# Kernel tuning notes

Hardware: AMD Instinct MI355X
Metric: run time of the kernel (lower is better)

The kernel has to match this reference:

```python
import jax, jax.numpy as jnp
import numpy as np

D_MODEL = 1024
N_HEADS = 16
D_K = D_MODEL // N_HEADS
B, T = 2, 2048


def setup_inputs() -> dict:
    key = jax.random.key(0)
    ks = jax.random.split(key, 9)
    s = 1.0 / np.sqrt(D_MODEL)
    def lin(kw, kb):
        W = jax.random.uniform(kw, (D_MODEL, D_MODEL), jnp.float32, -s, s)
        b = jax.random.uniform(kb, (D_MODEL,), jnp.float32, -s, s)
        return W, b
    Wq, bq = lin(ks[0], ks[1])
    Wk, bk = lin(ks[2], ks[3])
    Wv, bv = lin(ks[4], ks[5])
    Wo, bo = lin(ks[6], ks[7])
    x = jax.random.normal(ks[8], (B, T, D_MODEL), jnp.float32)
    return {"x": x, "Wq": Wq, "bq": bq, "Wk": Wk, "bk": bk,
            "Wv": Wv, "bv": bv, "Wo": Wo, "bo": bo}


def reference(x, Wq, bq, Wk, bk, Wv, bv, Wo, bo):
    Bn, Tn, _ = x.shape
    # torch Linear: x @ W.T + b
    def proj(W, b):
        y = x @ W.T + b  # [B, T, D]
        return y.reshape(Bn, Tn, N_HEADS, D_K).transpose(0, 2, 1, 3)  # [B, H, T, d_k]
    q = proj(Wq, bq)
    k = proj(Wk, bk)
    v = proj(Wv, bv)
    scores = jnp.einsum('bhqd,bhkd->bhqk', q, k) / jnp.sqrt(jnp.float32(D_K))
    causal = jnp.tril(jnp.ones((Tn, Tn), dtype=bool))  # True = keep
    scores = jnp.where(causal[None, None], scores, -jnp.inf)
    attn = jax.nn.softmax(scores, axis=-1)
    # dropout is identity in eval mode
    ctx = jnp.einsum('bhqk,bhkd->bhqd', attn, v)
    ctx = ctx.transpose(0, 2, 1, 3).reshape(Bn, Tn, D_MODEL)
    return ctx @ Wo.T + bo
```

## Files before the change

### kernel.cpp

```cpp
#include <hip/hip_runtime.h>
#include <hip/hip_bf16.h>
#include <stdint.h>

#define D_MODEL 1024
#define NH 16
#define DK 64
#define BB 2
#define TT 2048
#define NROWS (BB*TT)

typedef short bf16x8 __attribute__((ext_vector_type(8)));
typedef short bf16x4 __attribute__((ext_vector_type(4)));
typedef float f32x4  __attribute__((ext_vector_type(4)));

#if __has_builtin(__builtin_amdgcn_mfma_f32_16x16x16_bf16)
  #define MFMA16(a,b,c) __builtin_amdgcn_mfma_f32_16x16x16_bf16(a,b,c,0,0,0)
  #define HAVE_M16 1
#elif __has_builtin(__builtin_amdgcn_mfma_f32_16x16x16bf16_1k)
  #define MFMA16(a,b,c) __builtin_amdgcn_mfma_f32_16x16x16bf16_1k(a,b,c,0,0,0)
  #define HAVE_M16 1
#else
  #define HAVE_M16 0
#endif

#if __has_builtin(__builtin_amdgcn_global_load_lds)
  #define HAVE_GLDS 1
__device__ __forceinline__ void gload16(const unsigned short* g, unsigned short* lds){
    __builtin_amdgcn_global_load_lds(
        (const __attribute__((address_space(1))) unsigned int*)g,
        (__attribute__((address_space(3))) unsigned int*)lds, 16, 0, 0);
}
#else
  #define HAVE_GLDS 0
#endif

__device__ __forceinline__ unsigned pkbf(float a, float b){
    float2 t; t.x = a; t.y = b;
    __hip_bfloat162 h = __float22bfloat162_rn(t);
    return *reinterpret_cast<unsigned*>(&h);
}
__device__ __forceinline__ unsigned short bfbits(float a){
    __hip_bfloat16 h = __float2bfloat16(a);
    return *reinterpret_cast<unsigned short*>(&h);
}

__global__ __launch_bounds__(256) void conv_all(
    const float* __restrict__ x,
    const float* __restrict__ Wq, const float* __restrict__ Wk,
    const float* __restrict__ Wv, const float* __restrict__ Wo,
    unsigned short* __restrict__ xb, unsigned short* __restrict__ wb)
{
    const int blk = blockIdx.x;
    const float* src; unsigned short* dst; size_t i;
    if (blk < 2048) {
        src = x; dst = xb;
        i = ((size_t)blk * 256 + threadIdx.x) * 8;
    } else {
        const int t = (blk - 2048) >> 9;
        src = (t == 0) ? Wq : (t == 1) ? Wk : (t == 2) ? Wv : Wo;
        dst = wb + (size_t)t * D_MODEL * D_MODEL;
        i = ((size_t)((blk - 2048) & 511) * 256 + threadIdx.x) * 8;
    }
    float4 a = *(const float4*)(src + i);
    float4 b = *(const float4*)(src + i + 4);
    uint4 w;
    w.x = pkbf(a.x, a.y); w.y = pkbf(a.z, a.w);
    w.z = pkbf(b.x, b.y); w.w = pkbf(b.z, b.w);
    *(uint4*)(dst + i) = w;
}

__global__ __launch_bounds__(256) void conv_bf16(
    const float* __restrict__ x, unsigned short* __restrict__ y)
{
    size_t i = ((size_t)blockIdx.x * 256 + threadIdx.x) * 8;
    float4 a = *(const float4*)(x + i);
    float4 b = *(const float4*)(x + i + 4);
    uint4 w;
    w.x = pkbf(a.x, a.y); w.y = pkbf(a.z, a.w);
    w.z = pkbf(b.x, b.y); w.w = pkbf(b.z, b.w);
    *(uint4*)(y + i) = w;
}

#if HAVE_GLDS
template<int MI, int NB, bool CF32>
__device__ __forceinline__ void gemm_async(
    const unsigned short* __restrict__ Ap, const unsigned short* __restrict__ Bp,
    const float* __restrict__ bias, void* __restrict__ Cp,
    bool vt, float scale, unsigned short* As, unsigned short* Bs)
{
    constexpr int BMt = MI * 32, BNt = NB * 32;
    const int K = D_MODEL, N = D_MODEL;
    const int tid  = threadIdx.x;
    const int m0   = blockIdx.y * BMt;
    const int n0   = blockIdx.x * BNt;
    const int lane = tid & 63;
    const int w    = tid >> 6;
    const int wm   = (w >> 1) * (MI * 16);
    const int wn   = (w &  1) * (BNt / 2);
    const int l16  = lane & 15;
    const int quad = lane >> 4;
    const int crow = lane >> 2;
    const int ccol = (lane & 3) * 8;

    constexpr int CA = MI / 2;
    constexpr int CB = NB / 2;

    auto issue = [&](int buf, int k0){
        #pragma unroll
        for (int c = 0; c < CA; ++c) {
            const int chunk = w * CA + c;
            gload16(Ap + (size_t)(m0 + chunk*16 + crow) * K + k0 + ccol,
                    As + buf * BMt * 32 + chunk * 512);
        }
        #pragma unroll
        for (int c = 0; c < CB; ++c) {
            const int chunk = w * CB + c;
            gload16(Bp + (size_t)(n0 + chunk*16 + crow) * K + k0 + ccol,
                    Bs + buf * BNt * 32 + chunk * 512);
        }
    };

    f32x4 acc[MI][NB] = {};
    issue(0, 0);

    constexpr int ITER = D_MODEL / 32;
    for (int it = 0; it < ITER; ++it) {
        __syncthreads();
        if (it + 1 < ITER) issue((it + 1) & 1, (it + 1) * 32);
        const unsigned short* A = As + (it & 1) * BMt * 32;
        const unsigned short* B = Bs + (it & 1) * BNt * 32;
        bf16x8 af[MI], bg[NB];
        #pragma unroll
        for (int i = 0; i < MI; ++i)
            af[i] = *(const bf16x8*)&A[(wm + 16*i + l16) * 32 + quad * 8];
        #pragma unroll
        for (int j = 0; j < NB; ++j)
            bg[j] = *(const bf16x8*)&B[(wn + 16*j + l16) * 32 + quad * 8];
        #pragma unroll
        for (int i = 0; i < MI; ++i)
            #pragma unroll
            for (int j = 0; j < NB; ++j)
                acc[i][j] = __builtin_amdgcn_mfma_f32_16x16x32_bf16(af[i], bg[j], acc[i][j], 0, 0, 0);
    }

    #pragma unroll
    for (int j = 0; j < NB; ++j) {
        const int n = n0 + wn + 16*j + l16;
        const float bj = bias[n];
        #pragma unroll
        for (int i = 0; i < MI; ++i) {
            const int m = m0 + wm + 16*i + quad*4;
            if (vt) {
                const int b = m >> 11, t = m & 2047;
                ushort4 wv;
                wv.x = bfbits(acc[i][j][0] + bj);
                wv.y = bfbits(acc[i][j][1] + bj);
                wv.z = bfbits(acc[i][j][2] + bj);
                wv.w = bfbits(acc[i][j][3] + bj);
                *(ushort4*)((unsigned short*)Cp + (size_t)b * D_MODEL * TT
                            + (size_t)n * TT + t) = wv;
            } else {
                #pragma unroll
                for (int r = 0; r < 4; ++r) {
                    float v = (acc[i][j][r] + bj) * scale;
                    if (CF32) ((float*)Cp)[(size_t)(m + r) * N + n] = v;
                    else      ((__hip_bfloat16*)Cp)[(size_t)(m + r) * N + n] = __float2bfloat16(v);
                }
            }
        }
    }
}
#endif

#define ASTR 40

template<int MI, int NB, bool AF32, bool BF32, bool CF32>
__device__ __forceinline__ void gemm_body(
    const void* __restrict__ Ap, const void* __restrict__ Bp,
    const float* __restrict__ bias, void* __restrict__ Cp,
    bool vt, float scale, unsigned short* As, unsigned short* Bs)
{
    constexpr int BMt = MI * 32, BNt = NB * 32;
    const int K = D_MODEL, N = D_MODEL;
    const int tid  = threadIdx.x;
    const int m0   = blockIdx.y * BMt;
    const int n0   = blockIdx.x * BNt;
    const int lane = tid & 63;
    const int wave = tid >> 6;
    const int wm   = (wave >> 1) * (MI * 16);
    const int wn   = (wave &  1) * (BNt / 2);
    const int l16  = lane & 15;
    const int quad = lane >> 4;
    const int ar = (MI == 4) ? (tid >> 1) : (tid >> 2);
    const int ac = (MI == 4) ? ((tid & 1) * 16) : ((tid & 3) * 8);
    const int br = (NB == 4) ? (tid >> 1) : (tid >> 2);
    const int bc = (NB == 4) ? ((tid & 1) * 16) : ((tid & 3) * 8);

    uint4 pa[4], pb[4];

    auto loadA = [&](int k0){
        if (AF32) {
            const float* p = (const float*)Ap + (size_t)(m0 + ar) * K + k0 + ac;
            pa[0] = *(const uint4*)(p);     pa[1] = *(const uint4*)(p + 4);
            if (MI == 4) { pa[2] = *(const uint4*)(p + 8); pa[3] = *(const uint4*)(p + 12); }
        } else {
            const unsigned short* p = (const unsigned short*)Ap + (size_t)(m0 + ar) * K + k0 + ac;
            pa[0] = *(const uint4*)(p);
            if (MI == 4) pa[1] = *(const uint4*)(p + 8);
        }
    };
    auto loadB = [&](int k0){
        if (BF32) {
            const float* p = (const float*)Bp + (size_t)(n0 + br) * K + k0 + bc;
            pb[0] = *(const uint4*)(p); pb[1] = *(const uint4*)(p + 4);
            if (NB == 4) { pb[2] = *(const uint4*)(p + 8); pb[3] = *(const uint4*)(p + 12); }
        } else {
            const unsigned short* p = (const unsigned short*)Bp + (size_t)(n0 + br) * K + k0 + bc;
            pb[0] = *(const uint4*)(p);
            if (NB == 4) pb[1] = *(const uint4*)(p + 8);
        }
    };
    auto stage = [&](int buf){
        unsigned short* A = As + buf * BMt * ASTR;
        unsigned short* B = Bs + buf * BNt * ASTR;
        if (AF32) {
            const float* f = (const float*)pa;
            uint4 w0;
            w0.x = pkbf(f[0], f[1]); w0.y = pkbf(f[2], f[3]);
            w0.z = pkbf(f[4], f[5]); w0.w = pkbf(f[6], f[7]);
            *(uint4*)&A[ar*ASTR + ac] = w0;
            if (MI == 4) {
                uint4 w1;
                w1.x = pkbf(f[8], f[9]);   w1.y = pkbf(f[10], f[11]);
                w1.z = pkbf(f[12], f[13]); w1.w = pkbf(f[14], f[15]);
                *(uint4*)&A[ar*ASTR + ac + 8] = w1;
            }
        } else {
            *(uint4*)&A[ar*ASTR + ac] = pa[0];
            if (MI == 4) *(uint4*)&A[ar*ASTR + ac + 8] = pa[1];
        }
        if (BF32) {
            const float* g = (const float*)pb;
            uint4 v0;
            v0.x = pkbf(g[0], g[1]); v0.y = pkbf(g[2], g[3]);
            v0.z = pkbf(g[4], g[5]); v0.w = pkbf(g[6], g[7]);
            *(uint4*)&B[br*ASTR + bc] = v0;
            if (NB == 4) {
                uint4 v1;
                v1.x = pkbf(g[8], g[9]);   v1.y = pkbf(g[10], g[11]);
                v1.z = pkbf(g[12], g[13]); v1.w = pkbf(g[14], g[15]);
                *(uint4*)&B[br*ASTR + bc + 8] = v1;
            }
        } else {
            *(uint4*)&B[br*ASTR + bc] = pb[0];
            if (NB == 4) *(uint4*)&B[br*ASTR + bc + 8] = pb[1];
        }
    };

    f32x4 acc[MI][NB] = {};
    loadA(0); loadB(0);
    stage(0);

    constexpr int ITER = D_MODEL / 32;
    for (int it = 0; it < ITER; ++it) {
        __syncthreads();
        if (it + 1 < ITER) { loadA((it + 1) * 32); loadB((it + 1) * 32); }
        const unsigned short* A = As + (it & 1) * BMt * ASTR;
        const unsigned short* B = Bs + (it & 1) * BNt * ASTR;
        bf16x8 af[MI], bg[NB];
        #pragma unroll
        for (int i = 0; i < MI; ++i)
            af[i] = *(const bf16x8*)&A[(wm + 16*i + l16) * ASTR + quad * 8];
        #pragma unroll
        for (int j = 0; j < NB; ++j)
            bg[j] = *(const bf16x8*)&B[(wn + 16*j + l16) * ASTR + quad * 8];
        #pragma unroll
        for (int i = 0; i < MI; ++i)
            #pragma unroll
            for (int j = 0; j < NB; ++j)
                acc[i][j] = __builtin_amdgcn_mfma_f32_16x16x32_bf16(af[i], bg[j], acc[i][j], 0, 0, 0);
        if (it + 1 < ITER) stage((it + 1) & 1);
    }

    #pragma unroll
    for (int j = 0; j < NB; ++j) {
        const int n = n0 + wn + 16*j + l16;
        const float bj = bias[n];
        #pragma unroll
        for (int i = 0; i < MI; ++i) {
            const int m = m0 + wm + 16*i + quad*4;
            if (vt) {
                const int b = m >> 11, t = m & 2047;
                ushort4 wv;
                wv.x = bfbits(acc[i][j][0] + bj);
                wv.y = bfbits(acc[i][j][1] + bj);
                wv.z = bfbits(acc[i][j][2] + bj);
                wv.w = bfbits(acc[i][j][3] + bj);
                *(ushort4*)((unsigned short*)Cp + (size_t)b * D_MODEL * TT
                            + (size_t)n * TT + t) = wv;
            } else {
                #pragma unroll
                for (int r = 0; r < 4; ++r) {
                    float v = (acc[i][j][r] + bj) * scale;
                    if (CF32) ((float*)Cp)[(size_t)(m + r) * N + n] = v;
                    else      ((__hip_bfloat16*)Cp)[(size_t)(m + r) * N + n] = __float2bfloat16(v);
                }
            }
        }
    }
}

template<bool AF32, bool BF32>
__device__ __forceinline__ void qkv_sel(
    const void* x,
    const void* Wq, const float* bq, const void* Wk, const float* bk,
    const void* Wv, const float* bv,
    __hip_bfloat16* Qw, __hip_bfloat16* Kd, __hip_bfloat16* Vd,
    unsigned short* As, unsigned short* Bs)
{
    const void* W; const float* bi; void* C; bool vt = false; float sc = 1.0f;
    if      (blockIdx.z == 0) { W = Wq; bi = bq; C = Qw; sc = 0.125f; }
    else if (blockIdx.z == 1) { W = Wk; bi = bk; C = Kd; }
    else                      { W = Wv; bi = bv; C = Vd; vt = true; }
    gemm_body<4, 4, AF32, BF32, false>(x, W, bi, C, vt, sc, As, Bs);
}

#define QKV_KERNEL(name, AF, BF, XT)                                          \
__global__ __launch_bounds__(256, 3) void name(                               \
    const XT* __restrict__ x,                                                 \
    const void* __restrict__ Wq, const float* __restrict__ bq,                \
    const void* __restrict__ Wk, const float* __restrict__ bk,                \
    const void* __restrict__ Wv, const float* __restrict__ bv,                \
    __hip_bfloat16* __restrict__ Qw, __hip_bfloat16* __restrict__ Kd,         \
    __hip_bfloat16* __restrict__ Vd)                                          \
{                                                                             \
    __shared__ __align__(16) unsigned short As[2*128*ASTR];                   \
    __shared__ __align__(16) unsigned short Bs[2*128*ASTR];                   \
    qkv_sel<AF, BF>(x, Wq, bq, Wk, bk, Wv, bv, Qw, Kd, Vd, As, Bs);           \
}
QKV_KERNEL(gemm_qkv_f32, true,  true,  float)
QKV_KERNEL(gemm_qkv_xb,  false, true,  unsigned short)

__global__ __launch_bounds__(256, 3) void gemm_qkv_bb(
    const unsigned short* __restrict__ x,
    const unsigned short* __restrict__ Wq, const float* __restrict__ bq,
    const unsigned short* __restrict__ Wk, const float* __restrict__ bk,
    const unsigned short* __restrict__ Wv, const float* __restrict__ bv,
    __hip_bfloat16* __restrict__ Qw, __hip_bfloat16* __restrict__ Kd,
    __hip_bfloat16* __restrict__ Vd)
{
#if HAVE_GLDS
    __shared__ __align__(16) unsigned short As[2*128*32];
    __shared__ __align__(16) unsigned short Bs[2*128*32];
    const unsigned short* W; const float* bi; void* C; bool vt = false; float sc = 1.0f;
    if      (blockIdx.z == 0) { W = Wq; bi = bq; C = Qw; sc = 0.125f; }
    else if (blockIdx.z == 1) { W = Wk; bi = bk; C = Kd; }
    else                      { W = Wv; bi = bv; C = Vd; vt = true; }
    gemm_async<4, 4, false>(x, W, bi, C, vt, sc, As, Bs);
#else
    __shared__ __align__(16) unsigned short As[2*128*ASTR];
    __shared__ __align__(16) unsigned short Bs[2*128*ASTR];
    qkv_sel<false, false>(x, Wq, bq, Wk, bk, Wv, bv, Qw, Kd, Vd, As, Bs);
#endif
}

__global__ __launch_bounds__(256, 2) void gemm_out_f(
    const __hip_bfloat16* __restrict__ ctx, const void* __restrict__ Wo,
    const float* __restrict__ bo, float* __restrict__ out)
{
    __shared__ __align__(16) unsigned short As[2*128*ASTR];
    __shared__ __align__(16) unsigned short Bs[2*64*ASTR];
    gemm_body<4, 2, false, true, true>(ctx, Wo, bo, out, false, 1.0f, As, Bs);
}

__global__ __launch_bounds__(256, 2) void gemm_out_b(
    const __hip_bfloat16* __restrict__ ctx, const unsigned short* __restrict__ Wo,
    const float* __restrict__ bo, float* __restrict__ out)
{
#if HAVE_GLDS
    __shared__ __align__(16) unsigned short As[2*128*32];
    __shared__ __align__(16) unsigned short Bs[2*64*32];
    gemm_async<4, 2, true>((const unsigned short*)ctx, Wo, bo, out, false, 1.0f, As, Bs);
#else
    __shared__ __align__(16) unsigned short As[2*128*ASTR];
    __shared__ __align__(16) unsigned short Bs[2*64*ASTR];
    gemm_body<4, 2, false, false, true>(ctx, Wo, bo, out, false, 1.0f, As, Bs);
#endif
}

#define QSTR 68

__global__ __launch_bounds__(256, 3) void attn_mfma(
    const __hip_bfloat16* __restrict__ Q,
    const __hip_bfloat16* __restrict__ Km,
    const __hip_bfloat16* __restrict__ Vt,
    __hip_bfloat16* __restrict__ ctx)
{
    __shared__ __align__(16) unsigned short Ks [2][64*QSTR];
    __shared__ __align__(16) unsigned short VTs[2][64*QSTR];
    __shared__ __align__(16) unsigned short QP [64*QSTR];

    const int tid = threadIdx.x;
    const int blk = blockIdx.x;
    const int qt  = 31 - (blk & 31);
    const int h   = (blk >> 5) & 15;
    const int b   = blk >> 9;
    const int q0  = qt << 6;
    const size_t rowbase = (size_t)b * TT;
    const int colbase = h * DK;

    const int lane = tid & 63;
    const int w    = tid >> 6;
    const int l16  = lane & 15;
    const int quad = lane >> 4;
    const int lr = tid >> 2;
    const int lc = (tid & 3) << 4;

    const unsigned short* Vtb = (const unsigned short*)Vt + (size_t)b * D_MODEL * TT;

    uint4 kr0, kr1, vt0, vt1;
    auto prefetch = [&](int kv0){
        const unsigned short* pk = (const unsigned short*)Km +
            (rowbase + kv0 + lr) * D_MODEL + colbase + lc;
        kr0 = *(const uint4*)(pk);
        kr1 = *(const uint4*)(pk + 8);
        const unsigned short* pv = Vtb + (size_t)(colbase + lr) * TT + kv0 + lc;
        vt0 = *(const uint4*)(pv);
        vt1 = *(const uint4*)(pv + 8);
    };
    auto stageKV = [&](int buf){
        *(uint4*)&Ks [buf][lr*QSTR + lc]     = kr0;
        *(uint4*)&Ks [buf][lr*QSTR + lc + 8] = kr1;
        *(uint4*)&VTs[buf][lr*QSTR + lc]     = vt0;
        *(uint4*)&VTs[buf][lr*QSTR + lc + 8] = vt1;
    };

    {
        const unsigned short* p = (const unsigned short*)Q +
            (rowbase + q0 + lr) * D_MODEL + colbase + lc;
        *(uint4*)&QP[lr*QSTR + lc]     = *(const uint4*)(p);
        *(uint4*)&QP[lr*QSTR + lc + 8] = *(const uint4*)(p + 8);
    }
    prefetch(0);
    __syncthreads();
    bf16x8 af_q0 = *(const bf16x8*)&QP[(16*w + l16)*QSTR + quad*8];
    bf16x8 af_q1 = *(const bf16x8*)&QP[(16*w + l16)*QSTR + quad*8 + 32];
    stageKV(0);

#if HAVE_M16
    f32x4 o[4] = {};
    float lpart = 0.0f;

    for (int kt = 0; kt <= qt; ++kt) {
        __syncthreads();
        if (kt < qt) prefetch((kt + 1) << 6);
        const int cur = kt & 1;
        const bool diag = (kt == qt);

        f32x4 s[4] = {};
        #pragma unroll
        for (int cb = 0; cb < 4; ++cb) {
            bf16x8 ak0 = *(const bf16x8*)&Ks[cur][(16*cb + l16)*QSTR + quad*8];
            bf16x8 ak1 = *(const bf16x8*)&Ks[cur][(16*cb + l16)*QSTR + quad*8 + 32];
            s[cb] = __builtin_amdgcn_mfma_f32_16x16x32_bf16(ak0, af_q0, s[cb], 0, 0, 0);
            s[cb] = __builtin_amdgcn_mfma_f32_16x16x32_bf16(ak1, af_q1, s[cb], 0, 0, 0);
        }

        bf16x4 bp[4];
        #pragma unroll
        for (int cb = 0; cb < 4; ++cb) {
            float p[4];
            #pragma unroll
            for (int r = 0; r < 4; ++r) {
                float v = fminf(s[cb][r], 25.0f);
                bool keep = !diag || (16*cb + quad*4 + r <= 16*w + l16);
                p[r] = keep ? __expf(v) : 0.0f;
                lpart += p[r];
            }
            uint2 u; u.x = pkbf(p[0], p[1]); u.y = pkbf(p[2], p[3]);
            bp[cb] = *reinterpret_cast<bf16x4*>(&u);
        }

        #pragma unroll
        for (int nb = 0; nb < 4; ++nb)
            #pragma unroll
            for (int cb = 0; cb < 4; ++cb) {
                bf16x4 av = *(const bf16x4*)&VTs[cur][(16*nb + l16)*QSTR + 16*cb + quad*4];
                o[nb] = MFMA16(av, bp[cb], o[nb]);
            }

        if (kt < qt) stageKV((kt + 1) & 1);
    }

    lpart += __shfl_xor(lpart, 16);
    lpart += __shfl_xor(lpart, 32);
    const float inv_l = 1.0f / lpart;

    {
        const size_t row = (rowbase + q0 + 16*w + l16) * (size_t)D_MODEL + colbase;
        #pragma unroll
        for (int nb = 0; nb < 4; ++nb) {
            ushort4 wv;
            wv.x = bfbits(o[nb][0] * inv_l);
            wv.y = bfbits(o[nb][1] * inv_l);
            wv.z = bfbits(o[nb][2] * inv_l);
            wv.w = bfbits(o[nb][3] * inv_l);
            *(ushort4*)((unsigned short*)ctx + row + 16*nb + quad*4) = wv;
        }
    }
#else
    const short ob = (short)0x3F80;
    bf16x8 ones = { ob, ob, ob, ob, ob, ob, ob, ob };
    f32x4 o[4] = {};
    f32x4 l_acc = {};

    for (int kt = 0; kt <= qt; ++kt) {
        __syncthreads();
        if (kt < qt) prefetch((kt + 1) << 6);
        const int cur = kt & 1;

        f32x4 s[4] = {};
        #pragma unroll
        for (int cb = 0; cb < 4; ++cb) {
            bf16x8 bk0 = *(const bf16x8*)&Ks[cur][(16*cb + l16)*QSTR + quad*8];
            bf16x8 bk1 = *(const bf16x8*)&Ks[cur][(16*cb + l16)*QSTR + quad*8 + 32];
            s[cb] = __builtin_amdgcn_mfma_f32_16x16x32_bf16(af_q0, bk0, s[cb], 0, 0, 0);
            s[cb] = __builtin_amdgcn_mfma_f32_16x16x32_bf16(af_q1, bk1, s[cb], 0, 0, 0);
        }
        const bool diag = (kt == qt);
        #pragma unroll
        for (int cb = 0; cb < 4; ++cb)
            #pragma unroll
            for (int r = 0; r < 4; ++r) {
                float v = fminf(s[cb][r], 25.0f);
                float p = (diag && (16*cb + l16 > 16*w + quad*4 + r)) ? 0.0f : __expf(v);
                QP[(16*w + quad*4 + r)*QSTR + 16*cb + l16] = bfbits(p);
            }
        bf16x8 ap0 = *(const bf16x8*)&QP[(16*w + l16)*QSTR + quad*8];
        bf16x8 ap1 = *(const bf16x8*)&QP[(16*w + l16)*QSTR + quad*8 + 32];
        #pragma unroll
        for (int nb = 0; nb < 4; ++nb) {
            bf16x8 bv0 = *(const bf16x8*)&VTs[cur][(16*nb + l16)*QSTR + quad*8];
            bf16x8 bv1 = *(const bf16x8*)&VTs[cur][(16*nb + l16)*QSTR + quad*8 + 32];
            o[nb] = __builtin_amdgcn_mfma_f32_16x16x32_bf16(ap0, bv0, o[nb], 0, 0, 0);
            o[nb] = __builtin_amdgcn_mfma_f32_16x16x32_bf16(ap1, bv1, o[nb], 0, 0, 0);
        }
        l_acc = __builtin_amdgcn_mfma_f32_16x16x32_bf16(ap0, ones, l_acc, 0, 0, 0);
        l_acc = __builtin_amdgcn_mfma_f32_16x16x32_bf16(ap1, ones, l_acc, 0, 0, 0);
        if (kt < qt) stageKV((kt + 1) & 1);
    }
    float inv_l[4];
    #pragma unroll
    for (int r = 0; r < 4; ++r) inv_l[r] = 1.0f / l_acc[r];
    #pragma unroll
    for (int nb = 0; nb < 4; ++nb)
        #pragma unroll
        for (int r = 0; r < 4; ++r) {
            const int row = q0 + 16*w + quad*4 + r;
            ctx[(rowbase + row)*D_MODEL + colbase + 16*nb + l16] =
                __float2bfloat16(o[nb][r] * inv_l[r]);
        }
#endif
}

extern "C" void kernel_launch(void* const* d_in, const int* in_sizes, int n_in,
                              void* d_out, int out_size, void* d_ws, size_t ws_size,
                              hipStream_t stream) {
    const float* x  = (const float*)d_in[0];
    const float* Wq = (const float*)d_in[1];
    const float* bq = (const float*)d_in[2];
    const float* Wk = (const float*)d_in[3];
    const float* bk = (const float*)d_in[4];
    const float* Wv = (const float*)d_in[5];
    const float* bv = (const float*)d_in[6];
    const float* Wo = (const float*)d_in[7];
    const float* bo = (const float*)d_in[8];

    __hip_bfloat16* Qw = (__hip_bfloat16*)d_ws;
    __hip_bfloat16* Kd = (__hip_bfloat16*)d_out;
    __hip_bfloat16* Vd = Kd + (size_t)NROWS * D_MODEL;
    unsigned short* xb = (unsigned short*)d_ws + (size_t)NROWS * D_MODEL;
    unsigned short* wb = xb + (size_t)NROWS * D_MODEL;
    const size_t WSZ = (size_t)D_MODEL * D_MODEL;

    dim3 gqkv(D_MODEL / 128, NROWS / 128, 3);
    dim3 gout(D_MODEL / 64, NROWS / 128);
    const bool haveXB = ws_size >= (size_t)(16u << 20);
    const bool haveWB = ws_size >= (size_t)(24u << 20);

    if (haveWB) {
        conv_all<<<4096, 256, 0, stream>>>(x, Wq, Wk, Wv, Wo, xb, wb);
        gemm_qkv_bb<<<gqkv, 256, 0, stream>>>(xb, wb, bq, wb + WSZ, bk,
                                              wb + 2*WSZ, bv, Qw, Kd, Vd);
    } else if (haveXB) {
        conv_bf16<<<(NROWS * D_MODEL) / (256 * 8), 256, 0, stream>>>(x, xb);
        gemm_qkv_xb<<<gqkv, 256, 0, stream>>>(xb, Wq, bq, Wk, bk, Wv, bv, Qw, Kd, Vd);
    } else {
        gemm_qkv_f32<<<gqkv, 256, 0, stream>>>(x, Wq, bq, Wk, bk, Wv, bv, Qw, Kd, Vd);
    }

    attn_mfma<<<BB * NH * (TT / 64), 256, 0, stream>>>(Qw, Kd, Vd, Qw);

    if (haveWB)
        gemm_out_b<<<gout, 256, 0, stream>>>(Qw, wb + 3*WSZ, bo, (float*)d_out);
    else
        gemm_out_f<<<gout, 256, 0, stream>>>(Qw, Wo, bo, (float*)d_out);
}
```

Before: 202.6 us.

## Fold log2e into Q scale, use exp2, drop Q LDS staging, rebalance causal blocks

Scales Q by 0.125*log2(e) at projection so the attention softmax can use a hardware exp2 instead of __expf, and raises the clamp to keep the same range. Q fragments are loaded straight from global memory into registers, which removes the QP shared buffer and a barrier on the MFMA path. The diagonal mask check is split from the off-diagonal loop, launch bounds go to 4 blocks per CU, and the block index is remapped so consecutive blocks alternate long and short causal rows for load balance. The higher occupancy target may force register spilling.

```diff
diff --git a/kernel.cpp b/kernel.cpp
--- a/kernel.cpp
+++ b/kernel.cpp
@@ -8,6 +8,8 @@
 #define BB 2
 #define TT 2048
 #define NROWS (BB*TT)
+
+#define QSCALE 0.180336880f
 
 typedef short bf16x8 __attribute__((ext_vector_type(8)));
 typedef short bf16x4 __attribute__((ext_vector_type(4)));
@@ -33,6 +35,14 @@
 #else
   #define HAVE_GLDS 0
 #endif
+
+__device__ __forceinline__ float fexp2(float x){
+#if __has_builtin(__builtin_amdgcn_exp2f)
+    return __builtin_amdgcn_exp2f(x);
+#else
+    return exp2f(x);
+#endif
+}
 
 __device__ __forceinline__ unsigned pkbf(float a, float b){
     float2 t; t.x = a; t.y = b;
@@ -319,7 +329,7 @@
     unsigned short* As, unsigned short* Bs)
 {
     const void* W; const float* bi; void* C; bool vt = false; float sc = 1.0f;
-    if      (blockIdx.z == 0) { W = Wq; bi = bq; C = Qw; sc = 0.125f; }
+    if      (blockIdx.z == 0) { W = Wq; bi = bq; C = Qw; sc = QSCALE; }
     else if (blockIdx.z == 1) { W = Wk; bi = bk; C = Kd; }
     else                      { W = Wv; bi = bv; C = Vd; vt = true; }
     gemm_body<4, 4, AF32, BF32, false>(x, W, bi, C, vt, sc, As, Bs);
@@ -353,7 +363,7 @@
     __shared__ __align__(16) unsigned short As[2*128*32];
     __shared__ __align__(16) unsigned short Bs[2*128*32];
     const unsigned short* W; const float* bi; void* C; bool vt = false; float sc = 1.0f;
-    if      (blockIdx.z == 0) { W = Wq; bi = bq; C = Qw; sc = 0.125f; }
+    if      (blockIdx.z == 0) { W = Wq; bi = bq; C = Qw; sc = QSCALE; }
     else if (blockIdx.z == 1) { W = Wk; bi = bk; C = Kd; }
     else                      { W = Wv; bi = bv; C = Vd; vt = true; }
     gemm_async<4, 4, false>(x, W, bi, C, vt, sc, As, Bs);
@@ -390,7 +400,7 @@
 
 #define QSTR 68
 
-__global__ __launch_bounds__(256, 3) void attn_mfma(
+__global__ __launch_bounds__(256, 4) void attn_mfma(
     const __hip_bfloat16* __restrict__ Q,
     const __hip_bfloat16* __restrict__ Km,
     const __hip_bfloat16* __restrict__ Vt,
@@ -398,13 +408,18 @@
 {
     __shared__ __align__(16) unsigned short Ks [2][64*QSTR];
     __shared__ __align__(16) unsigned short VTs[2][64*QSTR];
-    __shared__ __align__(16) unsigned short QP [64*QSTR];
+#if !HAVE_M16
+    __shared__ __align__(16) unsigned short QP[64*QSTR];
+#endif
 
     const int tid = threadIdx.x;
     const int blk = blockIdx.x;
-    const int qt  = 31 - (blk & 31);
-    const int h   = (blk >> 5) & 15;
-    const int b   = blk >> 9;
+    const int i4 = blk & 255;
+    const int j4 = blk >> 8;
+    const int qt = (j4 & 1) ? (i4 & 31) : 31 - (i4 & 31);
+    const int bh = (i4 >> 5) + (j4 << 3);
+    const int b  = bh >> 4;
+    const int h  = bh & 15;
     const int q0  = qt << 6;
     const size_t rowbase = (size_t)b * TT;
     const int colbase = h * DK;
@@ -435,19 +450,15 @@
         *(uint4*)&VTs[buf][lr*QSTR + lc + 8] = vt1;
     };
 
-    {
-        const unsigned short* p = (const unsigned short*)Q +
-            (rowbase + q0 + lr) * D_MODEL + colbase + lc;
-        *(uint4*)&QP[lr*QSTR + lc]     = *(const uint4*)(p);
-        *(uint4*)&QP[lr*QSTR + lc + 8] = *(const uint4*)(p + 8);
-    }
+#if HAVE_M16
+    const unsigned short* qp = (const unsigned short*)Q +
+        (rowbase + q0 + 16*w + l16) * D_MODEL + colbase + quad*8;
+    bf16x8 af_q0 = *(const bf16x8*)(qp);
+    bf16x8 af_q1 = *(const bf16x8*)(qp + 32);
+
     prefetch(0);
-    __syncthreads();
-    bf16x8 af_q0 = *(const bf16x8*)&QP[(16*w + l16)*QSTR + quad*8];
-    bf16x8 af_q1 = *(const bf16x8*)&QP[(16*w + l16)*QSTR + quad*8 + 32];
     stageKV(0);
 
-#if HAVE_M16
     f32x4 o[4] = {};
     float lpart = 0.0f;
 
@@ -455,7 +466,6 @@
         __syncthreads();
         if (kt < qt) prefetch((kt + 1) << 6);
         const int cur = kt & 1;
-        const bool diag = (kt == qt);
 
         f32x4 s[4] = {};
         #pragma unroll
@@ -467,18 +477,32 @@
         }
 
         bf16x4 bp[4];
-        #pragma unroll
-        for (int cb = 0; cb < 4; ++cb) {
-            float p[4];
+        if (kt < qt) {
             #pragma unroll
-            for (int r = 0; r < 4; ++r) {
-                float v = fminf(s[cb][r], 25.0f);
-                bool keep = !diag || (16*cb + quad*4 + r <= 16*w + l16);
-                p[r] = keep ? __expf(v) : 0.0f;
-                lpart += p[r];
-            }
-            uint2 u; u.x = pkbf(p[0], p[1]); u.y = pkbf(p[2], p[3]);
-            bp[cb] = *reinterpret_cast<bf16x4*>(&u);
+            for (int cb = 0; cb < 4; ++cb) {
+                float p[4];
+                #pragma unroll
+                for (int r = 0; r < 4; ++r) {
+                    p[r] = fexp2(fminf(s[cb][r], 36.0f));
+                    lpart += p[r];
+                }
+                uint2 u; u.x = pkbf(p[0], p[1]); u.y = pkbf(p[2], p[3]);
+                bp[cb] = *reinterpret_cast<bf16x4*>(&u);
+            }
+        } else {
+            #pragma unroll
+            for (int cb = 0; cb < 4; ++cb) {
+                float p[4];
+                #pragma unroll
+                for (int r = 0; r < 4; ++r) {
+                    float v = fminf(s[cb][r], 36.0f);
+                    bool keep = (16*cb + quad*4 + r <= 16*w + l16);
+                    p[r] = keep ? fexp2(v) : 0.0f;
+                    lpart += p[r];
+                }
+                uint2 u; u.x = pkbf(p[0], p[1]); u.y = pkbf(p[2], p[3]);
+                bp[cb] = *reinterpret_cast<bf16x4*>(&u);
+            }
         }
 
         #pragma unroll
@@ -509,6 +533,18 @@
         }
     }
 #else
+    {
+        const unsigned short* p = (const unsigned short*)Q +
+            (rowbase + q0 + lr) * D_MODEL + colbase + lc;
+        *(uint4*)&QP[lr*QSTR + lc]     = *(const uint4*)(p);
+        *(uint4*)&QP[lr*QSTR + lc + 8] = *(const uint4*)(p + 8);
+    }
+    prefetch(0);
+    __syncthreads();
+    bf16x8 af_q0 = *(const bf16x8*)&QP[(16*w + l16)*QSTR + quad*8];
+    bf16x8 af_q1 = *(const bf16x8*)&QP[(16*w + l16)*QSTR + quad*8 + 32];
+    stageKV(0);
+
     const short ob = (short)0x3F80;
     bf16x8 ones = { ob, ob, ob, ob, ob, ob, ob, ob };
     f32x4 o[4] = {};
@@ -532,8 +568,8 @@
         for (int cb = 0; cb < 4; ++cb)
             #pragma unroll
             for (int r = 0; r < 4; ++r) {
-                float v = fminf(s[cb][r], 25.0f);
-                float p = (diag && (16*cb + l16 > 16*w + quad*4 + r)) ? 0.0f : __expf(v);
+                float v = fminf(s[cb][r], 36.0f);
+                float p = (diag && (16*cb + l16 > 16*w + quad*4 + r)) ? 0.0f : fexp2(v);
                 QP[(16*w + quad*4 + r)*QSTR + 16*cb + l16] = bfbits(p);
             }
         bf16x8 ap0 = *(const bf16x8*)&QP[(16*w + l16)*QSTR + quad*8];
```

Measured after the change: 188.5 us. 6.9% less time.
